# Optimization experiments

Measured on AMD Instinct MI355X. Metric: run time of the kernel, lower is better.

The kernel has to match this reference:

```python
import jax, jax.numpy as jnp
import numpy as np

ATTN_SCALE = 0.12
HEAD_DIM = 128


def _rms_norm(x):
    # F.rms_norm with no weight; eps defaults to machine eps of dtype
    eps = jnp.asarray(jnp.finfo(x.dtype).eps, x.dtype)
    return x * jax.lax.rsqrt(jnp.mean(x * x, axis=-1, keepdims=True) + eps)


def _rope(x):
    # x: [B, T, H, D]; standard rotary over (first-half, second-half) pairs
    T, D = x.shape[1], x.shape[-1]
    half = D // 2
    inv_freq = 1.0 / (10000.0 ** (jnp.arange(half, dtype=jnp.float32) / half))
    ang = jnp.arange(T, dtype=jnp.float32)[:, None] * inv_freq[None, :]  # [T, half]
    cos = jnp.cos(ang)[None, :, None, :].astype(x.dtype)
    sin = jnp.sin(ang)[None, :, None, :].astype(x.dtype)
    x1, x2 = x[..., :half], x[..., half:]
    return jnp.concatenate([x1 * cos - x2 * sin, x1 * sin + x2 * cos], axis=-1)


def setup_inputs() -> dict:
    key = jax.random.key(0)
    ks = jax.random.split(key, 4)
    B, T, dim, H, hd = 4, 2048, 1024, 8, HEAD_DIM
    hdim = H * hd
    std = 0.5 * dim ** (-0.5)
    bound = (3.0 ** 0.5) * std
    return {
        "x": jax.random.normal(ks[0], (B, T, dim), jnp.float32),
        "ve": jax.random.normal(ks[1], (B, T, hdim), jnp.float32),
        "qkv_w": jax.random.uniform(ks[2], (3, hdim, dim), jnp.float32, -bound, bound),
        "lambdas": jnp.array([0.5, 0.5], jnp.float32),
        "c_proj_w": jax.random.normal(ks[3], (dim, hdim), jnp.float32) * (hdim ** -0.5),
        "c_proj_b": jnp.zeros((dim,), jnp.float32),
    }


def reference(x, ve, qkv_w, lambdas, c_proj_w, c_proj_b):
    B, T, dim = x.shape
    hdim = qkv_w.shape[1]
    hd = HEAD_DIM
    H = hdim // hd
    # fused QKV projection: [B,T,3,H,hd]
    qkv = jnp.einsum('btd,ehd->bteh', x, qkv_w.reshape(3 * hdim, dim).reshape(3 * H, hd, dim).reshape(3 * hdim // hd, hd, dim))
    qkv = jnp.einsum('btd,fd->btf', x, qkv_w.reshape(3 * hdim, dim)).reshape(B, T, 3, H, hd)
    q, k, v = qkv[:, :, 0], qkv[:, :, 1], qkv[:, :, 2]  # each [B,T,H,hd]
    q, k = _rms_norm(q), _rms_norm(k)
    q, k = _rope(q), _rope(k)
    v = lambdas[0] * v + lambdas[1] * ve.reshape(B, T, H, hd)
    # causal SDPA with custom scale
    scores = jnp.einsum('bthd,bshd->bhts', q, k) * ATTN_SCALE  # [B,H,T,T]
    causal = jnp.tril(jnp.ones((T, T), dtype=bool))
    scores = jnp.where(causal[None, None], scores, jnp.finfo(scores.dtype).min)
    p = jax.nn.softmax(scores, axis=-1)
    y = jnp.einsum('bhts,bshd->bthd', p, v).reshape(B, T, hdim)
    return y @ c_proj_w.T + c_proj_b
```

## Files before the change

### kernel.cpp

```cpp
#include <hip/hip_runtime.h>
#include <math.h>

typedef unsigned short u16;
typedef short bf16x8 __attribute__((ext_vector_type(8)));
typedef u16 u16x2 __attribute__((ext_vector_type(2)));
typedef u16 u16x4 __attribute__((ext_vector_type(4)));
typedef u16 u16x8 __attribute__((ext_vector_type(8)));
typedef float f32x2 __attribute__((ext_vector_type(2)));
typedef float f32x4 __attribute__((ext_vector_type(4)));
typedef float f32x16 __attribute__((ext_vector_type(16)));

typedef __attribute__((address_space(1))) const void gvoid_t;
typedef __attribute__((address_space(3))) void lvoid_t;

__device__ __forceinline__ u16 f2bf(float f) {
  union { float f; unsigned u; } v; v.f = f;
  unsigned r = v.u + 0x7fffu + ((v.u >> 16) & 1u);
  return (u16)(r >> 16);
}
__device__ __forceinline__ float bf2f(u16 h) {
  union { unsigned u; float f; } v; v.u = ((unsigned)h) << 16;
  return v.f;
}
__device__ __forceinline__ f32x4 mfma16(bf16x8 a, bf16x8 b, f32x4 c) {
  return __builtin_amdgcn_mfma_f32_16x16x32_bf16(a, b, c, 0, 0, 0);
}
__device__ __forceinline__ f32x16 mfma32(bf16x8 a, bf16x8 b, f32x16 c) {
  return __builtin_amdgcn_mfma_f32_32x32x16_bf16(a, b, c, 0, 0, 0);
}
__device__ __forceinline__ void gload_lds16(const void* g, void* l) {
  __builtin_amdgcn_global_load_lds((gvoid_t*)g, (lvoid_t*)l, 16, 0, 0);
}
__device__ __forceinline__ unsigned cvtpk_bf16(float lo, float hi) {
  unsigned r;
  asm("v_cvt_pk_bf16_f32 %0, %1, %2" : "=v"(r) : "v"(lo), "v"(hi));
  return r;
}
__device__ __forceinline__ void pswap32(unsigned& a, unsigned& b) {
  asm("v_permlane32_swap_b32 %0, %1" : "+v"(a), "+v"(b));
}

#if __has_builtin(__builtin_amdgcn_exp2f)
#define EXPW(x) __builtin_amdgcn_exp2f(x)
#define SCALE_W 0.17312354f
#define DEFER_THR 11.5415603f
#else
#define EXPW(x) __expf(x)
#define SCALE_W 0.12f
#define DEFER_THR 8.0f
#endif

#define BAR() __builtin_amdgcn_s_barrier()
#define WAITLGKM()                          \
  asm volatile("s_waitcnt lgkmcnt(0)");     \
  __builtin_amdgcn_sched_barrier(0)
#define WAITVMC(N)                                    \
  do {                                                \
    __builtin_amdgcn_s_waitcnt(0x0F70 | (N));         \
    __builtin_amdgcn_sched_barrier(0);                \
  } while (0)

__global__ __launch_bounds__(256) void cvt_bf16_kernel(const float* __restrict__ in,
                                                       u16* __restrict__ out, int n4) {
  int i = blockIdx.x * 256 + threadIdx.x;
  if (i >= n4) return;
  f32x4 v = *(const f32x4*)(in + (size_t)i * 4);
  u16x4 o;
  o[0] = f2bf(v[0]); o[1] = f2bf(v[1]); o[2] = f2bf(v[2]); o[3] = f2bf(v[3]);
  *(u16x4*)(out + (size_t)i * 4) = o;
}

__global__ __launch_bounds__(256) void rope_tab_kernel(float* __restrict__ ct,
                                                       float* __restrict__ st) {
  int i = blockIdx.x * 256 + threadIdx.x;
  int t = i >> 6, j = i & 63;
  float inv = powf(10000.f, -(float)j * (1.0f / 64.0f));
  float ang = (float)t * inv;
  ct[i] = cosf(ang);
  st[i] = sinf(ang);
}

__global__ __launch_bounds__(512, 1) void gemm192_kernel(
    const u16* __restrict__ A, const u16* __restrict__ B, u16* __restrict__ C,
    int M, int N, int K, int nbn) {
  constexpr int WM = 128;
  constexpr int MI = 4;
  constexpr int NI = 3;
  constexpr int AR = 4;
  constexpr int NR = 7;
  __shared__ u16 Alds[2][256 * 64];
  __shared__ u16 Blds[2][192 * 64];
  int nwg = gridDim.x;
  int cpx = nwg >> 3;
  int bid = blockIdx.x;
  int swz = (bid & 7) * cpx + (bid >> 3);
  int bm = (swz & 3) + 4 * (swz / (4 * nbn));
  int bn = (swz >> 2) % nbn;
  size_t m0 = (size_t)bm * 256, n0 = (size_t)bn * 192;
  int tid = threadIdx.x, wid = tid >> 6, lane = tid & 63;
  int wr = wid >> 2, wc = wid & 3, l15 = lane & 15, l4 = lane >> 4;
  int srow = tid >> 3, sch = tid & 7;

  const u16* Abase = A + m0 * K;
  const u16* Bbase = B + n0 * K;

  f32x4 acc[8][NI];
#pragma unroll
  for (int m = 0; m < 8; m++)
#pragma unroll
    for (int n = 0; n < NI; n++) acc[m][n] = f32x4{0.f, 0.f, 0.f, 0.f};

  auto stageR = [&](int buf, int kt, int r) {
    if (r < AR) {
      int row = 64 * r + srow;
      gload_lds16(Abase + (size_t)row * K + kt * 64 + 8 * (sch ^ (row & 7)),
                  &Alds[buf][(64 * r + 8 * wid) * 64]);
    } else {
      int row = 64 * (r - AR) + srow;
      gload_lds16(Bbase + (size_t)row * K + kt * 64 + 8 * (sch ^ (row & 7)),
                  &Blds[buf][(64 * (r - AR) + 8 * wid) * 64]);
    }
  };
  auto rdA = [&](int buf, int half, bf16x8 (&a)[MI][2]) {
#pragma unroll
    for (int mi = 0; mi < MI; ++mi)
#pragma unroll
      for (int kk = 0; kk < 2; ++kk) {
        int row = WM * wr + 64 * half + 16 * mi + l15;
        a[mi][kk] = *(const bf16x8*)((const char*)(&Alds[buf][0]) + row * 128 +
                                     ((kk * 64 + 16 * l4) ^ ((row & 7) << 4)));
      }
  };
  auto rdB = [&](int buf, bf16x8 (&bb)[NI][2]) {
#pragma unroll
    for (int ni = 0; ni < NI; ++ni)
#pragma unroll
      for (int kk = 0; kk < 2; ++kk) {
        int row = 48 * wc + 16 * ni + l15;
        bb[ni][kk] = *(const bf16x8*)((const char*)(&Blds[buf][0]) + row * 128 +
                                      ((kk * 64 + 16 * l4) ^ ((row & 7) << 4)));
      }
  };

#define HALFM(AF, BF, QM)                                                 \
  do {                                                                    \
    __builtin_amdgcn_s_setprio(1);                                        \
    _Pragma("unroll") for (int mi = 0; mi < MI; ++mi)                     \
        _Pragma("unroll") for (int ni = 0; ni < NI; ++ni)                 \
            _Pragma("unroll") for (int kk = 0; kk < 2; ++kk)              \
                acc[4 * QM + mi][ni] =                                    \
        mfma16(AF[mi][kk], BF[ni][kk], acc[4 * QM + mi][ni]);             \
    __builtin_amdgcn_s_setprio(0);                                        \
  } while (0)

#pragma unroll
  for (int r = 0; r < NR; ++r) stageR(0, 0, r);
  WAITVMC(0);
  BAR();

  int nk = K >> 6;
  bf16x8 a[MI][2], b[NI][2];
  for (int t = 0; t < nk; ++t) {
    int buf = t & 1, nxt = buf ^ 1;
    bool pf = (t + 1 < nk);
    rdA(buf, 0, a);
    rdB(buf, b);
    if (pf) { stageR(nxt, t + 1, 0); stageR(nxt, t + 1, 1); stageR(nxt, t + 1, 2); stageR(nxt, t + 1, 3); }
    BAR();
    WAITLGKM();
    HALFM(a, b, 0);
    BAR();
    rdA(buf, 1, a);
    if (pf) { stageR(nxt, t + 1, 4); stageR(nxt, t + 1, 5); stageR(nxt, t + 1, 6); }
    BAR();
    WAITLGKM();
    HALFM(a, b, 1);
    WAITVMC(0);
    BAR();
  }

#pragma unroll
  for (int mi = 0; mi < 8; ++mi) {
#pragma unroll
    for (int ni = 0; ni < NI; ++ni) {
      size_t row = m0 + WM * wr + 16 * mi + 4 * l4;
      size_t col = n0 + 48 * wc + 16 * ni + l15;
#pragma unroll
      for (int i = 0; i < 4; ++i) {
        C[(row + i) * N + col] = f2bf(acc[mi][ni][i]);
      }
    }
  }
#undef HALFM
}

template <int BM, int OUTF32>
__global__ __launch_bounds__(512, 1) void gemm4p_kernel(
    const u16* __restrict__ A, const u16* __restrict__ B, void* __restrict__ C,
    const float* __restrict__ bias, int M, int N, int K, int nbn) {
  constexpr int WM = BM / 2;
  constexpr int MI = (WM / 32 > 0) ? WM / 32 : 1;
  constexpr int NACC = 2 * MI;
  constexpr int AR = BM / 64;
  constexpr int NR = AR + 4;
  constexpr int R0 = (NR + 2) / 3;
  constexpr int R1 = R0 + (NR - R0 + 1) / 2;
  __shared__ u16 Alds[2][BM * 64];
  __shared__ u16 Blds[2][256 * 64];
  int nwg = gridDim.x;
  int cpx = nwg >> 3;
  int bid = blockIdx.x;
  int swz = (bid & 7) * cpx + (bid >> 3);
  int bm = (swz & 3) + 4 * (swz / (4 * nbn));
  int bn = (swz >> 2) % nbn;
  size_t m0 = (size_t)bm * BM, n0 = (size_t)bn * 256;
  int tid = threadIdx.x, wid = tid >> 6, lane = tid & 63;
  int wr = wid >> 2, wc = wid & 3, l15 = lane & 15, l4 = lane >> 4;
  int srow = tid >> 3, sch = tid & 7;

  const u16* Abase = A + m0 * K;
  const u16* Bbase = B + n0 * K;

  f32x4 acc[NACC][4];
#pragma unroll
  for (int m = 0; m < NACC; m++)
#pragma unroll
    for (int n = 0; n < 4; n++) acc[m][n] = f32x4{0.f, 0.f, 0.f, 0.f};

  auto stageR = [&](int buf, int kt, int r) {
    if (r < AR) {
      int row = 64 * r + srow;
      gload_lds16(Abase + (size_t)row * K + kt * 64 + 8 * (sch ^ (row & 7)),
                  &Alds[buf][(64 * r + 8 * wid) * 64]);
    } else {
      int row = 64 * (r - AR) + srow;
      gload_lds16(Bbase + (size_t)row * K + kt * 64 + 8 * (sch ^ (row & 7)),
                  &Blds[buf][(64 * (r - AR) + 8 * wid) * 64]);
    }
  };
  auto rdA = [&](int buf, int qm, bf16x8 (&a)[MI][2]) {
#pragma unroll
    for (int mi = 0; mi < MI; ++mi)
#pragma unroll
      for (int kk = 0; kk < 2; ++kk) {
        int row = WM * wr + (WM / 2) * qm + 16 * mi + l15;
        a[mi][kk] = *(const bf16x8*)((const char*)(&Alds[buf][0]) + row * 128 +
                                     ((kk * 64 + 16 * l4) ^ ((row & 7) << 4)));
      }
  };
  auto rdB = [&](int buf, int qn, bf16x8 (&bb)[2][2]) {
#pragma unroll
    for (int ni = 0; ni < 2; ++ni)
#pragma unroll
      for (int kk = 0; kk < 2; ++kk) {
        int row = 64 * wc + 32 * qn + 16 * ni + l15;
        bb[ni][kk] = *(const bf16x8*)((const char*)(&Blds[buf][0]) + row * 128 +
                                      ((kk * 64 + 16 * l4) ^ ((row & 7) << 4)));
      }
  };

#define QUADX(AF, BF, QM, QN)                                             \
  do {                                                                    \
    __builtin_amdgcn_s_setprio(1);                                        \
    _Pragma("unroll") for (int mi = 0; mi < MI; ++mi)                     \
        _Pragma("unroll") for (int ni = 0; ni < 2; ++ni)                  \
            _Pragma("unroll") for (int kk = 0; kk < 2; ++kk)              \
                acc[MI * QM + mi][2 * QN + ni] =                          \
        mfma16(AF[mi][kk], BF[ni][kk], acc[MI * QM + mi][2 * QN + ni]);   \
    __builtin_amdgcn_s_setprio(0);                                        \
  } while (0)

#pragma unroll
  for (int r = 0; r < NR; ++r) stageR(0, 0, r);
  WAITVMC(0);
  BAR();

  int nk = K >> 6;
  bf16x8 a[MI][2], b0[2][2], b1[2][2];
  for (int t = 0; t < nk; ++t) {
    int buf = t & 1, nxt = buf ^ 1;
    bool pf = (t + 1 < nk);
    rdA(buf, 0, a);
    rdB(buf, 0, b0);
    if (pf) {
#pragma unroll
      for (int r = 0; r < R0; ++r) stageR(nxt, t + 1, r);
    }
    BAR();
    WAITLGKM();
    QUADX(a, b0, 0, 0);
    BAR();
    rdB(buf, 1, b1);
    if (pf) {
#pragma unroll
      for (int r = R0; r < R1; ++r) stageR(nxt, t + 1, r);
    }
    BAR();
    WAITLGKM();
    QUADX(a, b1, 0, 1);
    BAR();
    rdA(buf, 1, a);
    if (pf) {
#pragma unroll
      for (int r = R1; r < NR; ++r) stageR(nxt, t + 1, r);
    }
    BAR();
    WAITLGKM();
    QUADX(a, b0, 1, 0);
    BAR();
    QUADX(a, b1, 1, 1);
    WAITVMC(0);
    BAR();
  }

#pragma unroll
  for (int mi = 0; mi < NACC; ++mi) {
#pragma unroll
    for (int ni = 0; ni < 4; ++ni) {
      size_t row = m0 + WM * wr + 16 * mi + 4 * l4;
      size_t col = n0 + 64 * wc + 16 * ni + l15;
#pragma unroll
      for (int i = 0; i < 4; ++i) {
        float v = acc[mi][ni][i];
        if constexpr (OUTF32) {
          ((float*)C)[(row + i) * N + col] = v + bias[col];
        } else {
          ((u16*)C)[(row + i) * N + col] = f2bf(v);
        }
      }
    }
  }
#undef QUADX
}

__global__ __launch_bounds__(256) void transform_kernel(
    const u16* __restrict__ qkv, const float* __restrict__ ve,
    const float* __restrict__ lam, const float* __restrict__ ct,
    const float* __restrict__ st, u16* __restrict__ qn, u16* __restrict__ kn,
    u16* __restrict__ vt) {
  constexpr int T = 2048;
  __shared__ u16 vtile[64][136];
  int tt = blockIdx.x, bh = blockIdx.y;
  int b = bh >> 3, h = bh & 7;
  int tid = threadIdx.x, wid = tid >> 6, lane = tid & 63;
  int lsub = lane & 15, lrow = lane >> 4;
  float l0 = lam[0], l1 = lam[1];
  int d0 = 8 * lsub;
  float sgn = (lsub < 8) ? -1.f : 1.f;
  int jj = d0 & 63;
#pragma unroll
  for (int it = 0; it < 4; ++it) {
    int tl = wid * 16 + it * 4 + lrow;
    int t = tt * 64 + tl;
    size_t base = ((size_t)(b * T + t)) * 3072 + h * 128 + d0;
    u16x8 qraw = *(const u16x8*)(qkv + base);
    u16x8 kraw = *(const u16x8*)(qkv + base + 1024);
    u16x8 vraw = *(const u16x8*)(qkv + base + 2048);
    const float* vep = ve + ((size_t)(b * T + t)) * 1024 + h * 128 + d0;
    f32x4 ve0 = *(const f32x4*)(vep);
    f32x4 ve1 = *(const f32x4*)(vep + 4);
    float q[8], k[8];
    float sq = 0.f, sk = 0.f;
#pragma unroll
    for (int i = 0; i < 8; ++i) {
      q[i] = bf2f(qraw[i]); k[i] = bf2f(kraw[i]);
      sq += q[i] * q[i]; sk += k[i] * k[i];
    }
#pragma unroll
    for (int m = 1; m < 16; m <<= 1) {
      sq += __shfl_xor(sq, m);
      sk += __shfl_xor(sk, m);
    }
    float qs = rsqrtf(sq * (1.f / 128.f) + 1.1920929e-7f);
    float ks = rsqrtf(sk * (1.f / 128.f) + 1.1920929e-7f);
#pragma unroll
    for (int i = 0; i < 8; ++i) { q[i] *= qs; k[i] *= ks; }
    f32x4 c0 = *(const f32x4*)(ct + t * 64 + jj);
    f32x4 c1 = *(const f32x4*)(ct + t * 64 + jj + 4);
    f32x4 s0 = *(const f32x4*)(st + t * 64 + jj);
    f32x4 s1 = *(const f32x4*)(st + t * 64 + jj + 4);
    u16x8 oq, ok, ov;
#pragma unroll
    for (int i = 0; i < 8; ++i) {
      float qp = __shfl_xor(q[i], 8), kp = __shfl_xor(k[i], 8);
      float cc = (i < 4) ? c0[i & 3] : c1[i & 3];
      float ss = (i < 4) ? s0[i & 3] : s1[i & 3];
      oq[i] = f2bf(q[i] * cc + sgn * qp * ss);
      ok[i] = f2bf(k[i] * cc + sgn * kp * ss);
      float vv = (i < 4) ? ve0[i & 3] : ve1[i & 3];
      ov[i] = f2bf(l0 * bf2f(vraw[i]) + l1 * vv);
    }
    size_t orow = ((size_t)bh * T + t) * 128 + d0;
    *(u16x8*)(qn + orow) = oq;
    *(u16x8*)(kn + orow) = ok;
    *(u16x8*)&vtile[tl][d0] = ov;
  }
  __syncthreads();
#pragma unroll
  for (int it = 0; it < 4; ++it) {
    int ci = it * 256 + tid;
    int d = ci >> 3, c8 = ci & 7;
    u16x8 o;
#pragma unroll
    for (int u = 0; u < 8; u++) o[u] = vtile[c8 * 8 + u][d];
    *(u16x8*)(vt + ((size_t)bh * 128 + d) * T + tt * 64 + c8 * 8) = o;
  }
}

__global__ __launch_bounds__(512, 2) void attn_kernel(
    const u16* __restrict__ Qn, const u16* __restrict__ Kn,
    const u16* __restrict__ Vt, u16* __restrict__ Y) {
  constexpr int T = 2048;
  __shared__ u16 Klds[2][64 * 128];
  __shared__ u16 Vlds[2][128 * 64];
  int bid = blockIdx.x;
  int s = bid >> 5;
  int bh = bid & 31;
  int b = bh >> 3, h = bh & 7;
  int tid = threadIdx.x, wid = tid >> 6, lane = tid & 63;
  int l31 = lane & 31, hh = lane >> 5;
  const u16* Qb = Qn + (size_t)bh * T * 128;
  const u16* Kb = Kn + (size_t)bh * T * 128;
  const u16* Vb = Vt + (size_t)bh * 128 * T;
  int q0w = s * 256 + wid * 32;
  int qmaxw = q0w + 31;
  int ktend = 4 * s + 4;
  int qg = q0w + l31;

  bf16x8 qf[8];
  {
    const u16* qr = Qb + (size_t)(q0w + l31) * 128 + 8 * hh;
#pragma unroll
    for (int ks = 0; ks < 8; ks++) qf[ks] = *(const bf16x8*)(qr + 16 * ks);
  }
  f32x16 acc[4];
#pragma unroll
  for (int mt = 0; mt < 4; mt++)
#pragma unroll
    for (int r = 0; r < 16; r++) acc[mt][r] = 0.f;
  float m_run = -1e30f, l_run = 0.f;

  auto stage = [&](int buf, int kt) {
#pragma unroll
    for (int it = 0; it < 2; ++it) {
      int id = it * 512 + tid;
      int r = id >> 4, c = id & 15;
      gload_lds16(Kb + (size_t)(kt * 64 + r) * 128 + 8 * (c ^ (r & 7)),
                  &Klds[buf][(size_t)(it * 512 + (tid & ~63)) * 8]);
      int rv = id >> 3, cv = id & 7;
      gload_lds16(Vb + (size_t)rv * T + kt * 64 + 8 * (cv ^ (rv & 7)),
                  &Vlds[buf][(size_t)(it * 512 + (tid & ~63)) * 8]);
    }
  };

  stage(0, 0);

  for (int kt = 0; kt < ktend; ++kt) {
    int cur = kt & 1;
    if (kt + 1 < ktend) {
      stage(cur ^ 1, kt + 1);
      WAITVMC(4);
    } else {
      WAITVMC(0);
    }
    BAR();
    if (kt * 64 <= qmaxw) {
      const char* kb = (const char*)&Klds[cur][0];
      const char* vb = (const char*)&Vlds[cur][0];
      int rswz = (l31 & 7) << 4;
      f32x16 st0, st1;
#pragma unroll
      for (int r = 0; r < 16; r++) { st0[r] = 0.f; st1[r] = 0.f; }
      __builtin_amdgcn_s_setprio(1);
#pragma unroll
      for (int ks = 0; ks < 8; ks++) {
        bf16x8 kf0 = *(const bf16x8*)(kb + ((l31 * 256 + 32 * ks + 16 * hh) ^ rswz));
        bf16x8 kf1 = *(const bf16x8*)(kb + (((32 + l31) * 256 + 32 * ks + 16 * hh) ^ rswz));
        st0 = mfma32(kf0, qf[ks], st0);
        st1 = mfma32(kf1, qf[ks], st1);
      }
      __builtin_amdgcn_s_setprio(0);
      bool edge = (kt == (qmaxw >> 6));
      if (edge) {
#pragma unroll
        for (int r = 0; r < 16; r++) {
          int kvb = kt * 64 + (r & 3) + 8 * (r >> 2) + 4 * hh;
          if (kvb > qg) st0[r] = -1e30f;
          if (kvb + 32 > qg) st1[r] = -1e30f;
        }
      }
      float m8[8];
#pragma unroll
      for (int r = 0; r < 8; r++)
        m8[r] = fmaxf(fmaxf(st0[r], st0[r + 8]), fmaxf(st1[r], st1[r + 8]));
#pragma unroll
      for (int r = 0; r < 4; r++) m8[r] = fmaxf(m8[r], m8[r + 4]);
      float pm = fmaxf(fmaxf(m8[0], m8[1]), fmaxf(m8[2], m8[3]));
      pm = fmaxf(pm, __shfl_xor(pm, 32));
      float pmn = pm * SCALE_W;
      bool nos = __all(pmn <= m_run + DEFER_THR);
      float mnew = nos ? m_run : fmaxf(m_run, pmn);
      if (!nos) {
        float alpha = EXPW(m_run - mnew);
        l_run *= alpha;
#pragma unroll
        for (int mt = 0; mt < 4; mt++)
#pragma unroll
          for (int r = 0; r < 16; r++) acc[mt][r] *= alpha;
        m_run = mnew;
      }
      float sa = 0.f, sb = 0.f, sc = 0.f, sd = 0.f;
#pragma unroll
      for (int r = 0; r < 4; r++) {
        st0[r]      = EXPW(fmaf(st0[r],      SCALE_W, -mnew)); sa += st0[r];
        st0[r + 4]  = EXPW(fmaf(st0[r + 4],  SCALE_W, -mnew)); sb += st0[r + 4];
        st0[r + 8]  = EXPW(fmaf(st0[r + 8],  SCALE_W, -mnew)); sc += st0[r + 8];
        st0[r + 12] = EXPW(fmaf(st0[r + 12], SCALE_W, -mnew)); sd += st0[r + 12];
        st1[r]      = EXPW(fmaf(st1[r],      SCALE_W, -mnew)); sa += st1[r];
        st1[r + 4]  = EXPW(fmaf(st1[r + 4],  SCALE_W, -mnew)); sb += st1[r + 4];
        st1[r + 8]  = EXPW(fmaf(st1[r + 8],  SCALE_W, -mnew)); sc += st1[r + 8];
        st1[r + 12] = EXPW(fmaf(st1[r + 12], SCALE_W, -mnew)); sd += st1[r + 12];
      }
      float ps = (sa + sb) + (sc + sd);
      ps += __shfl_xor(ps, 32);
      l_run += ps;
      unsigned pA0[4], pB0[4], pA1[4], pB1[4];
#pragma unroll
      for (int rr = 0; rr < 4; rr++) {
        pA0[rr] = cvtpk_bf16(st0[4 * rr], st0[4 * rr + 1]);
        pB0[rr] = cvtpk_bf16(st0[4 * rr + 2], st0[4 * rr + 3]);
        pA1[rr] = cvtpk_bf16(st1[4 * rr], st1[4 * rr + 1]);
        pB1[rr] = cvtpk_bf16(st1[4 * rr + 2], st1[4 * rr + 3]);
      }
      bf16x8 pf[4];
#pragma unroll
      for (int ks2 = 0; ks2 < 4; ks2++) {
        int k1 = ks2 & 1;
        unsigned a0, b0, a1, b1;
        if (ks2 < 2) { a0 = pA0[2 * k1]; b0 = pA0[2 * k1 + 1]; a1 = pB0[2 * k1]; b1 = pB0[2 * k1 + 1]; }
        else         { a0 = pA1[2 * k1]; b0 = pA1[2 * k1 + 1]; a1 = pB1[2 * k1]; b1 = pB1[2 * k1 + 1]; }
        pswap32(a0, b0);
        pswap32(a1, b1);
        union { unsigned w[4]; bf16x8 v; } u;
        u.w[0] = a0; u.w[1] = a1; u.w[2] = b0; u.w[3] = b1;
        pf[ks2] = u.v;
      }
      __builtin_amdgcn_s_setprio(1);
#pragma unroll
      for (int mt = 0; mt < 4; mt++) {
        int row = 32 * mt + l31;
#pragma unroll
        for (int ks2 = 0; ks2 < 4; ks2++) {
          bf16x8 vf = *(const bf16x8*)(vb + ((row * 128 + 32 * ks2 + 16 * hh) ^ rswz));
          acc[mt] = mfma32(vf, pf[ks2], acc[mt]);
        }
      }
      __builtin_amdgcn_s_setprio(0);
    }
    BAR();
  }
  float linv = 1.f / l_run;
  size_t yrow = (size_t)b * T + q0w + l31;
  u16* yp = Y + yrow * 1024 + h * 128;
#pragma unroll
  for (int mt = 0; mt < 4; mt++) {
#pragma unroll
    for (int rr = 0; rr < 4; rr++) {
      u16x4 o;
#pragma unroll
      for (int i = 0; i < 4; i++) o[i] = f2bf(acc[mt][4 * rr + i] * linv);
      *(u16x4*)(yp + 32 * mt + 8 * rr + 4 * hh) = o;
    }
  }
}

extern "C" void kernel_launch(void* const* d_in, const int* in_sizes, int n_in,
                              void* d_out, int out_size, void* d_ws, size_t ws_size,
                              hipStream_t stream) {
  (void)in_sizes; (void)n_in; (void)out_size; (void)ws_size;
  const float* x = (const float*)d_in[0];
  const float* ve = (const float*)d_in[1];
  const float* qkvw = (const float*)d_in[2];
  const float* lam = (const float*)d_in[3];
  const float* cpw = (const float*)d_in[4];
  const float* cpb = (const float*)d_in[5];
  float* out = (float*)d_out;
  char* ws = (char*)d_ws;

  u16* xb   = (u16*)(ws + 0);
  u16* wqkv = (u16*)(ws + 16777216);
  u16* wp   = (u16*)(ws + 23068672);
  u16* qkv  = (u16*)(ws + 25165824);
  u16* qn   = (u16*)(ws + 75497472);
  u16* kn   = (u16*)(ws + 92274688);
  u16* vt   = (u16*)(ws + 109051904);
  float* ctab = (float*)(ws + 125829120);
  float* stab = (float*)(ws + 126353408);
  u16* y = xb;

  rope_tab_kernel<<<512, 256, 0, stream>>>(ctab, stab);
  cvt_bf16_kernel<<<8192, 256, 0, stream>>>(x, xb, 2097152);
  cvt_bf16_kernel<<<3072, 256, 0, stream>>>(qkvw, wqkv, 786432);
  cvt_bf16_kernel<<<1024, 256, 0, stream>>>(cpw, wp, 262144);
  gemm192_kernel<<<512, 512, 0, stream>>>(xb, wqkv, qkv, 8192, 3072, 1024, 16);
  transform_kernel<<<dim3(32, 32), 256, 0, stream>>>(qkv, ve, lam, ctab, stab, qn, kn, vt);
  attn_kernel<<<256, 512, 0, stream>>>(qn, kn, vt, y);
  gemm4p_kernel<64, 1><<<512, 512, 0, stream>>>(y, wp, out, cpb, 8192, 1024, 1024, 4);
}
```

Baseline: 208.1 us.

## Split long causal attention rows into KV halves with a merge kernel

The attention kernel moves from 256 blocks of 512 threads (256 query rows each) to 768 blocks of 256 threads (128 query rows each). A constant schedule table orders blocks longest-first, and the query tiles with the most key blocks (tiles 8-15) are split into two KV halves. Split halves write unnormalized bf16 partial outputs plus running max and sum to workspace, and a new merge kernel combines them with log-sum-exp weights. The aim is better load balance and occupancy across CUs for causal work. The cost is an extra launch, partial-output traffic, and some precision loss from storing partials in bf16.

```diff
diff --git a/kernel.cpp b/kernel.cpp
--- a/kernel.cpp
+++ b/kernel.cpp
@@ -59,6 +59,9 @@
     __builtin_amdgcn_s_waitcnt(0x0F70 | (N));         \
     __builtin_amdgcn_sched_barrier(0);                \
   } while (0)
+
+__constant__ int C_ST[24] = {15,15,7,14,14,13,13,6,12,12,11,11,5,10,10,4,9,9,8,8,3,2,1,0};
+__constant__ int C_HF[24] = {0,1,-1,0,1,0,1,-1,0,1,0,1,-1,0,1,-1,0,1,0,1,-1,-1,-1,-1};
 
 __global__ __launch_bounds__(256) void cvt_bf16_kernel(const float* __restrict__ in,
                                                        u16* __restrict__ out, int n4) {
@@ -407,24 +410,28 @@
   }
 }
 
-__global__ __launch_bounds__(512, 2) void attn_kernel(
+__global__ __launch_bounds__(256, 2) void attn_kernel(
     const u16* __restrict__ Qn, const u16* __restrict__ Kn,
-    const u16* __restrict__ Vt, u16* __restrict__ Y) {
+    const u16* __restrict__ Vt, u16* __restrict__ Y,
+    u16* __restrict__ pO, float* __restrict__ pml) {
   constexpr int T = 2048;
   __shared__ u16 Klds[2][64 * 128];
   __shared__ u16 Vlds[2][128 * 64];
   int bid = blockIdx.x;
-  int s = bid >> 5;
+  int c = bid >> 5;
   int bh = bid & 31;
+  int st = C_ST[c];
+  int half = C_HF[c];
+  int kt0 = (half == 1) ? st + 1 : 0;
+  int kt1 = (half == 0) ? st + 1 : 2 * st + 2;
   int b = bh >> 3, h = bh & 7;
   int tid = threadIdx.x, wid = tid >> 6, lane = tid & 63;
   int l31 = lane & 31, hh = lane >> 5;
   const u16* Qb = Qn + (size_t)bh * T * 128;
   const u16* Kb = Kn + (size_t)bh * T * 128;
   const u16* Vb = Vt + (size_t)bh * 128 * T;
-  int q0w = s * 256 + wid * 32;
+  int q0w = st * 128 + wid * 32;
   int qmaxw = q0w + 31;
-  int ktend = 4 * s + 4;
   int qg = q0w + l31;
 
   bf16x8 qf[8];
@@ -442,24 +449,26 @@
 
   auto stage = [&](int buf, int kt) {
 #pragma unroll
-    for (int it = 0; it < 2; ++it) {
-      int id = it * 512 + tid;
-      int r = id >> 4, c = id & 15;
-      gload_lds16(Kb + (size_t)(kt * 64 + r) * 128 + 8 * (c ^ (r & 7)),
-                  &Klds[buf][(size_t)(it * 512 + (tid & ~63)) * 8]);
+    for (int it = 0; it < 4; ++it) {
+      int id = wid * 256 + it * 64 + lane;
+      int r = id >> 4, cc = id & 15;
+      gload_lds16(Kb + (size_t)(kt * 64 + r) * 128 + 8 * (cc ^ (r & 7)),
+                  &Klds[buf][(size_t)(wid * 256 + it * 64) * 8]);
       int rv = id >> 3, cv = id & 7;
       gload_lds16(Vb + (size_t)rv * T + kt * 64 + 8 * (cv ^ (rv & 7)),
-                  &Vlds[buf][(size_t)(it * 512 + (tid & ~63)) * 8]);
+                  &Vlds[buf][(size_t)(wid * 256 + it * 64) * 8]);
     }
   };
 
-  stage(0, 0);
-
-  for (int kt = 0; kt < ktend; ++kt) {
-    int cur = kt & 1;
-    if (kt + 1 < ktend) {
+  int nsteps = kt1 - kt0;
+  stage(0, kt0);
+
+  for (int j = 0; j < nsteps; ++j) {
+    int kt = kt0 + j;
+    int cur = j & 1;
+    if (j + 1 < nsteps) {
       stage(cur ^ 1, kt + 1);
-      WAITVMC(4);
+      WAITVMC(8);
     } else {
       WAITVMC(0);
     }
@@ -559,18 +568,67 @@
     }
     BAR();
   }
-  float linv = 1.f / l_run;
-  size_t yrow = (size_t)b * T + q0w + l31;
-  u16* yp = Y + yrow * 1024 + h * 128;
-#pragma unroll
-  for (int mt = 0; mt < 4; mt++) {
-#pragma unroll
-    for (int rr = 0; rr < 4; rr++) {
-      u16x4 o;
-#pragma unroll
-      for (int i = 0; i < 4; i++) o[i] = f2bf(acc[mt][4 * rr + i] * linv);
-      *(u16x4*)(yp + 32 * mt + 8 * rr + 4 * hh) = o;
-    }
+  if (half < 0) {
+    float linv = 1.f / l_run;
+    size_t yrow = (size_t)b * T + q0w + l31;
+    u16* yp = Y + yrow * 1024 + h * 128;
+#pragma unroll
+    for (int mt = 0; mt < 4; mt++) {
+#pragma unroll
+      for (int rr = 0; rr < 4; rr++) {
+        u16x4 o;
+#pragma unroll
+        for (int i = 0; i < 4; i++) o[i] = f2bf(acc[mt][4 * rr + i] * linv);
+        *(u16x4*)(yp + 32 * mt + 8 * rr + 4 * hh) = o;
+      }
+    }
+  } else {
+    int pidx = (((st - 8) << 5) + bh) * 2 + half;
+    int qrow = wid * 32 + l31;
+    u16* po = pO + (size_t)pidx * 16384 + (size_t)qrow * 128;
+#pragma unroll
+    for (int mt = 0; mt < 4; mt++) {
+#pragma unroll
+      for (int rr = 0; rr < 4; rr++) {
+        u16x4 o;
+#pragma unroll
+        for (int i = 0; i < 4; i++) o[i] = f2bf(acc[mt][4 * rr + i]);
+        *(u16x4*)(po + 32 * mt + 8 * rr + 4 * hh) = o;
+      }
+    }
+    if (hh == 0) {
+      pml[pidx * 256 + qrow] = m_run;
+      pml[pidx * 256 + 128 + qrow] = l_run;
+    }
+  }
+}
+
+__global__ __launch_bounds__(256) void attn_merge_kernel(
+    const u16* __restrict__ pO, const float* __restrict__ pml,
+    u16* __restrict__ Y) {
+  int blk = blockIdx.x;
+  int st = 8 + (blk >> 5), bh = blk & 31;
+  int b = bh >> 3, h = bh & 7;
+  int tid = threadIdx.x;
+  int row = tid >> 1, dh = tid & 1;
+  int base = blk * 2;
+  const u16* o1 = pO + (size_t)base * 16384 + (size_t)row * 128 + dh * 64;
+  const u16* o2 = o1 + 16384;
+  float m1 = pml[base * 256 + row], l1 = pml[base * 256 + 128 + row];
+  float m2 = pml[(base + 1) * 256 + row], l2 = pml[(base + 1) * 256 + 128 + row];
+  float m = fmaxf(m1, m2);
+  float w1 = EXPW(m1 - m), w2 = EXPW(m2 - m);
+  float inv = 1.f / (w1 * l1 + w2 * l2);
+  w1 *= inv; w2 *= inv;
+  u16* yp = Y + ((size_t)b * 2048 + 128 * st + row) * 1024 + h * 128 + dh * 64;
+#pragma unroll
+  for (int i = 0; i < 8; ++i) {
+    u16x8 a = *(const u16x8*)(o1 + 8 * i);
+    u16x8 cvec = *(const u16x8*)(o2 + 8 * i);
+    u16x8 o;
+#pragma unroll
+    for (int j = 0; j < 8; ++j) o[j] = f2bf(w1 * bf2f(a[j]) + w2 * bf2f(cvec[j]));
+    *(u16x8*)(yp + 8 * i) = o;
   }
 }
 
@@ -597,6 +655,8 @@
   float* ctab = (float*)(ws + 125829120);
   float* stab = (float*)(ws + 126353408);
   u16* y = xb;
+  u16* pO = qkv;
+  float* pml = (float*)(ws + 25165824 + 16777216);
 
   rope_tab_kernel<<<512, 256, 0, stream>>>(ctab, stab);
   cvt_bf16_kernel<<<8192, 256, 0, stream>>>(x, xb, 2097152);
@@ -604,6 +664,7 @@
   cvt_bf16_kernel<<<1024, 256, 0, stream>>>(cpw, wp, 262144);
   gemm192_kernel<<<512, 512, 0, stream>>>(xb, wqkv, qkv, 8192, 3072, 1024, 16);
   transform_kernel<<<dim3(32, 32), 256, 0, stream>>>(qkv, ve, lam, ctab, stab, qn, kn, vt);
-  attn_kernel<<<256, 512, 0, stream>>>(qn, kn, vt, y);
+  attn_kernel<<<768, 256, 0, stream>>>(qn, kn, vt, y, pO, pml);
+  attn_merge_kernel<<<256, 256, 0, stream>>>(pO, pml, y);
   gemm4p_kernel<64, 1><<<512, 512, 0, stream>>>(y, wp, out, cpb, 8192, 1024, 1024, 4);
 }
```

Result: faster. 203.7 us (-2.1%).
